# Performance work log

Hardware: AMD Instinct MI355X
Metric: run time of the kernel (lower is better)

Reference implementation:

```python
import jax, jax.numpy as jnp
import numpy as np

B, C, H, W = 16, 256, 32, 32
LN_EPS = 1e-5


def setup_inputs() -> dict:
    key = jax.random.key(0)
    ks = jax.random.split(key, 12)
    s = 1.0 / np.sqrt(C)
    x = jax.random.normal(ks[0], (B, C, H, W), dtype=jnp.float32)
    # Linear weights stored as [in, out] (torch stores [out, in]; math is x @ W_in_out + b)
    wq = jax.random.uniform(ks[1], (C, C), jnp.float32, -s, s)
    bq = jax.random.uniform(ks[2], (C,), jnp.float32, -s, s)
    wk = jax.random.uniform(ks[3], (C, C), jnp.float32, -s, s)
    bk = jax.random.uniform(ks[4], (C,), jnp.float32, -s, s)
    wv = jax.random.uniform(ks[5], (C, C), jnp.float32, -s, s)
    bv = jax.random.uniform(ks[6], (C,), jnp.float32, -s, s)
    w1 = jax.random.uniform(ks[7], (C, C), jnp.float32, -s, s)
    b1 = jax.random.uniform(ks[8], (C,), jnp.float32, -s, s)
    w2 = jax.random.uniform(ks[9], (C, C), jnp.float32, -s, s)
    b2 = jax.random.uniform(ks[10], (C,), jnp.float32, -s, s)
    gamma = jnp.ones((C,), jnp.float32)
    beta = jnp.zeros((C,), jnp.float32)
    return {"x": x, "wq": wq, "bq": bq, "wk": wk, "bk": bk, "wv": wv, "bv": bv,
            "w1": w1, "b1": b1, "w2": w2, "b2": b2, "gamma": gamma, "beta": beta}


def reference(x, wq, bq, wk, bk, wv, bv, w1, b1, w2, b2, gamma, beta):
    Bd, Cd, Hd, Wd = x.shape
    t = x.reshape(Bd, Cd, Hd * Wd).transpose(0, 2, 1)  # [B, N, C]
    q = t @ wq + bq
    k = t @ wk + bk
    v = t @ wv + bv
    # matrix[b,i,j] = q[b,i,:] . k[b,j,:]  (no 1/sqrt(d) scaling, as in source)
    m = jnp.einsum('bic,bjc->bij', q, k)
    # softmax over dim=-2 (the query axis i)
    m = jax.nn.softmax(m, axis=-2)
    # att[b,j,c] = sum_i v[b,i,c] * m[b,i,j]  (v^T @ m, then permute)
    att = jnp.einsum('bic,bij->bjc', v, m)  # [B, N, C]
    # MLP (SiLU, hidden = C), dropout p=0 -> identity; DropPath eval -> identity
    att = jax.nn.silu(att @ w1 + b1) @ w2 + b2
    # LayerNorm over channel dim
    mu = jnp.mean(att, axis=-1, keepdims=True)
    var = jnp.var(att, axis=-1, keepdims=True)
    att = (att - mu) * jax.lax.rsqrt(var + LN_EPS) * gamma + beta
    return att.transpose(0, 2, 1).reshape(Bd, Cd, Hd, Wd)
```

## Files before the change

### kernel.cpp

```cpp
#include <hip/hip_runtime.h>

#define BB 16
#define CC 256
#define NN 1024

typedef _Float16 f16;
typedef __attribute__((ext_vector_type(8))) _Float16 half8;
typedef __attribute__((ext_vector_type(4))) float f32x4;

__device__ __forceinline__ half8 ldg8(const f16* p) {
  return *reinterpret_cast<const half8*>(p);
}

__device__ __forceinline__ void gll16(const f16* g, f16* l) {
  __builtin_amdgcn_global_load_lds((const __attribute__((address_space(1))) void*)g,
                                   (__attribute__((address_space(3))) void*)l, 16, 0, 0);
}

#define VMCNT(n) asm volatile("s_waitcnt vmcnt(" #n ")" ::: "memory")
#define BAR() __builtin_amdgcn_s_barrier()

__device__ __forceinline__ void stage64k(const f16* __restrict__ g, f16* l, int wave, int lane) {
#pragma unroll
  for (int k = 0; k < 16; ++k) {
    int ob = k * 2048 + wave * 512;
    gll16(g + ob + lane * 8, l + ob);
  }
}

__device__ __forceinline__ void stage64k8(const f16* __restrict__ g, f16* l, int wave, int lane) {
#pragma unroll
  for (int k = 0; k < 8; ++k) {
    int ob = k * 4096 + wave * 512;
    gll16(g + ob + lane * 8, l + ob);
  }
}

struct WP5 {
  const float* s[5];
  f16* d[5];
};

__global__ void __launch_bounds__(256) k_packW(WP5 p) {
  __shared__ float ws[256][17];
  int m = blockIdx.y, ct = blockIdx.x;
  const float* W = p.s[m];
  f16* wp = p.d[m];
  int tid = threadIdx.x;
  int col = tid & 15, cig = tid >> 4;
#pragma unroll
  for (int pg = 0; pg < 16; ++pg) {
    int ci = pg * 16 + cig;
    ws[ci][col] = W[(size_t)ci * 256 + ct * 16 + col];
  }
  __syncthreads();
  int lane = tid & 63, wave = tid >> 6;
  int row16 = lane & 15, quad = lane >> 4;
#pragma unroll
  for (int kk = 0; kk < 2; ++kk) {
    int kc = wave * 2 + kk;
    half8 o;
#pragma unroll
    for (int j = 0; j < 8; ++j) o[j] = (f16)ws[kc * 32 + quad * 8 + j][row16];
    *reinterpret_cast<half8*>(wp + ((size_t)ct * 8 + kc) * 512 + lane * 8) = o;
  }
}

struct QkvSmem {
  union {
    struct { f16 hi[32][264]; f16 lo[32][264]; } ts;
    f16 ex[2][16][264];
    f16 exv[256][40];
  };
};

__global__ void __launch_bounds__(256) k_qkv(const float* __restrict__ x,
    const f16* __restrict__ wqp, const f16* __restrict__ wkp, const f16* __restrict__ wvp,
    const float* __restrict__ bq, const float* __restrict__ bk, const float* __restrict__ bv,
    f16* __restrict__ qp, f16* __restrict__ kp, f16* __restrict__ vp, int b_base) {
  __shared__ QkvSmem sm;
  int bl = blockIdx.x, bg = b_base + bl, n0 = blockIdx.y * 32;
  int tid = threadIdx.x, wave = tid >> 6, lane = tid & 63;
  int row16 = lane & 15, quad = lane >> 4;
  int g = wave >> 1, h = wave & 1;

#pragma unroll
  for (int e = tid; e < 2048; e += 256) {
    int c = e >> 3, n4 = (e & 7) << 2;
    float4 u = *reinterpret_cast<const float4*>(x + (size_t)(bg * CC + c) * NN + n0 + n4);
    float uv[4] = {u.x, u.y, u.z, u.w};
#pragma unroll
    for (int i = 0; i < 4; ++i) {
      f16 hh = (f16)uv[i];
      sm.ts.hi[n4 + i][c] = hh;
      sm.ts.lo[n4 + i][c] = (f16)(uv[i] - (float)hh);
    }
  }
  __syncthreads();

  half8 ah[8], al[8];
#pragma unroll
  for (int kc = 0; kc < 8; ++kc) {
    ah[kc] = *reinterpret_cast<const half8*>(&sm.ts.hi[g * 16 + row16][kc * 32 + quad * 8]);
    al[kc] = *reinterpret_cast<const half8*>(&sm.ts.lo[g * 16 + row16][kc * 32 + quad * 8]);
  }
  __syncthreads();

  const f16* WTs[2]    = {wqp, wkp};
  const float* biases[2] = {bq, bk};
  f16* outs[2]         = {qp, kp};
#pragma unroll
  for (int z = 0; z < 2; ++z) {
    const f16* WT = WTs[z];
    const float* bias = biases[z];
    f16* outp = outs[z];
#pragma unroll
    for (int cp = 0; cp < 2; ++cp) {
      f32x4 acch[4], accl[4];
#pragma unroll
      for (int u = 0; u < 4; ++u) { acch[u] = {0.f,0.f,0.f,0.f}; accl[u] = {0.f,0.f,0.f,0.f}; }
#pragma unroll
      for (int kc = 0; kc < 8; ++kc) {
#pragma unroll
        for (int u = 0; u < 4; ++u) {
          int ct = h * 8 + cp * 4 + u;
          half8 b = ldg8(WT + ((size_t)ct * 8 + kc) * 512 + lane * 8);
          acch[u] = __builtin_amdgcn_mfma_f32_16x16x32_f16(ah[kc], b, acch[u], 0, 0, 0);
          accl[u] = __builtin_amdgcn_mfma_f32_16x16x32_f16(al[kc], b, accl[u], 0, 0, 0);
        }
      }
#pragma unroll
      for (int u = 0; u < 4; ++u) {
        int ct = h * 8 + cp * 4 + u;
        int co = ct * 16 + row16;
        float bb = bias[co];
#pragma unroll
        for (int r = 0; r < 4; ++r)
          sm.ex[g][quad * 4 + r][co] = (f16)(acch[u][r] + accl[u][r] + bb);
      }
    }
    const f16* exr = &sm.ex[g][row16][0];
    size_t fb = ((size_t)bl * 64 + (n0 >> 4) + g) * 8;
#pragma unroll
    for (int k = 0; k < 4; ++k) {
      int kc = h * 4 + k;
      half8 hv = *reinterpret_cast<const half8*>(exr + kc * 32 + quad * 8);
      *reinterpret_cast<half8*>(outp + (fb + kc) * 512 + lane * 8) = hv;
    }
  }
  __syncthreads();

#pragma unroll
  for (int cp = 0; cp < 2; ++cp) {
    f32x4 acch[4], accl[4];
#pragma unroll
    for (int u = 0; u < 4; ++u) { acch[u] = {0.f,0.f,0.f,0.f}; accl[u] = {0.f,0.f,0.f,0.f}; }
#pragma unroll
    for (int kc = 0; kc < 8; ++kc) {
#pragma unroll
      for (int u = 0; u < 4; ++u) {
        int ct = h * 8 + cp * 4 + u;
        half8 b = ldg8(wvp + ((size_t)ct * 8 + kc) * 512 + lane * 8);
        acch[u] = __builtin_amdgcn_mfma_f32_16x16x32_f16(ah[kc], b, acch[u], 0, 0, 0);
        accl[u] = __builtin_amdgcn_mfma_f32_16x16x32_f16(al[kc], b, accl[u], 0, 0, 0);
      }
    }
#pragma unroll
    for (int u = 0; u < 4; ++u) {
      int ct = h * 8 + cp * 4 + u;
      int co = ct * 16 + row16;
      float bb = bv[co];
#pragma unroll
      for (int r = 0; r < 4; ++r)
        sm.exv[co][g * 16 + quad * 4 + r] = (f16)(acch[u][r] + accl[u][r] + bb);
    }
  }
  __syncthreads();
  size_t vb = ((size_t)bl * 32 + blockIdx.y) * 16;
#pragma unroll
  for (int f = 0; f < 4; ++f) {
    int ct = wave * 4 + f;
    half8 o = *reinterpret_cast<const half8*>(&sm.exv[ct * 16 + row16][quad * 8]);
    *reinterpret_cast<half8*>(vp + (vb + ct) * 512 + lane * 8) = o;
  }
}

struct AttnSmem {
  union {
    struct {
      f16 QB[2][64 * 256];
      f16 VB[2][64 * 256];
    } s;
    struct {
      union {
        float Ocmb[4][16][260];
        f16 ex2[4][16][264];
      } a;
      f16 ex[4][16][264];
    } e;
  } u;
  f16 P[8][2][16][40];
  float ml[8][2][16];
  float lnbuf[8][2][16];
};

__global__ void __launch_bounds__(512, 2) k_attn_mlp(
    const f16* __restrict__ qp, const f16* __restrict__ kp, const f16* __restrict__ vp,
    const f16* __restrict__ w1p, const float* __restrict__ b1,
    const f16* __restrict__ w2p, const float* __restrict__ b2,
    const float* __restrict__ gamma, const float* __restrict__ beta,
    float* __restrict__ out, int b_base) {
  __shared__ AttnSmem sm;
  int bl = blockIdx.x, bg = b_base + bl;
  int j0 = blockIdx.y * 64;
  int tid = threadIdx.x, wave = tid >> 6, lane = tid & 63;
  int row16 = lane & 15, quad = lane >> 4;
  int jt_l = wave & 3, p = wave >> 2;
  int jw = j0 + jt_l * 16;

  const f16* kbase = kp + (size_t)bl * NN * CC;
  int jt = (j0 >> 4) + jt_l;
  half8 kf[8];
#pragma unroll
  for (int kc = 0; kc < 8; ++kc)
    kf[kc] = ldg8(kbase + ((size_t)jt * 8 + kc) * 512 + lane * 8);

  const f16* qbase = qp + (size_t)bl * NN * CC;
  const f16* vbase = vp + (size_t)bl * CC * NN;

  stage64k8(qbase, &sm.u.s.QB[0][0], wave, lane);
  stage64k8(vbase, &sm.u.s.VB[0][0], wave, lane);
  VMCNT(8);
  BAR();

  f32x4 O[16];
#pragma unroll
  for (int ct = 0; ct < 16; ++ct) O[ct] = {0.f, 0.f, 0.f, 0.f};
  float m_run[4], l_lane[4];
#pragma unroll
  for (int r = 0; r < 4; ++r) { m_run[r] = -1e30f; l_lane[r] = 0.f; }

  const f16* QBp = &sm.u.s.QB[p][0];
  const f16* VBp = &sm.u.s.VB[p][0];

  for (int it = 0; it < 8; ++it) {
    f32x4 s[4];
#pragma unroll
    for (int f = 0; f < 4; ++f) s[f] = {0.f, 0.f, 0.f, 0.f};
#pragma unroll
    for (int kc = 0; kc < 8; ++kc) {
#pragma unroll
      for (int f = 0; f < 4; ++f) {
        half8 b = *reinterpret_cast<const half8*>(&QBp[(f * 8 + kc) * 512 + lane * 8]);
        s[f] = __builtin_amdgcn_mfma_f32_16x16x32_f16(kf[kc], b, s[f], 0, 0, 0);
      }
    }
    BAR();
    stage64k8(qbase + (size_t)((it + 1) & 7) * 32768, &sm.u.s.QB[0][0], wave, lane);

    float alpha[4];
#pragma unroll
    for (int r = 0; r < 4; ++r) {
      float mx = s[0][r];
#pragma unroll
      for (int f = 1; f < 4; ++f) mx = fmaxf(mx, s[f][r]);
#pragma unroll
      for (int off = 1; off < 16; off <<= 1) mx = fmaxf(mx, __shfl_xor(mx, off, 64));
      float mnew = fmaxf(m_run[r], mx);
      alpha[r] = __expf(m_run[r] - mnew);
      m_run[r] = mnew;
      float ps = 0.f;
#pragma unroll
      for (int f = 0; f < 4; ++f) {
        float pv = __expf(s[f][r] - mnew);
        ps += pv;
        sm.P[wave][f >> 1][quad * 4 + r][(f & 1) * 16 + row16] = (f16)pv;
      }
      l_lane[r] = l_lane[r] * alpha[r] + ps;
    }
#pragma unroll
    for (int ct = 0; ct < 16; ++ct)
#pragma unroll
      for (int r = 0; r < 4; ++r) O[ct][r] *= alpha[r];

    VMCNT(8);
    BAR();

#pragma unroll
    for (int c4 = 0; c4 < 2; ++c4) {
      half8 pf = *reinterpret_cast<const half8*>(&sm.P[wave][c4][row16][quad * 8]);
#pragma unroll
      for (int ct = 0; ct < 16; ++ct) {
        half8 vf = *reinterpret_cast<const half8*>(&VBp[(c4 * 16 + ct) * 512 + lane * 8]);
        O[ct] = __builtin_amdgcn_mfma_f32_16x16x32_f16(pf, vf, O[ct], 0, 0, 0);
      }
    }
    BAR();
    stage64k8(vbase + (size_t)((it + 1) & 7) * 32768, &sm.u.s.VB[0][0], wave, lane);
    VMCNT(8);
    BAR();
  }
  VMCNT(0);
  BAR();

#pragma unroll
  for (int r = 0; r < 4; ++r) {
#pragma unroll
    for (int off = 1; off < 16; off <<= 1) l_lane[r] += __shfl_xor(l_lane[r], off, 64);
  }
  if (row16 == 0) {
#pragma unroll
    for (int r = 0; r < 4; ++r) {
      sm.ml[wave][0][quad * 4 + r] = m_run[r];
      sm.ml[wave][1][quad * 4 + r] = l_lane[r];
    }
  }
  BAR();

  int partner = wave ^ 4;
  float alphaS[4], invL[4];
#pragma unroll
  for (int r = 0; r < 4; ++r) {
    int j = quad * 4 + r;
    float ma = m_run[r], mb = sm.ml[partner][0][j];
    float M = fmaxf(ma, mb);
    float la = l_lane[r], lb = sm.ml[partner][1][j];
    float L = la * __expf(ma - M) + lb * __expf(mb - M);
    alphaS[r] = __expf(ma - M);
    invL[r] = 1.f / L;
  }
#pragma unroll
  for (int ct = 0; ct < 16; ++ct)
#pragma unroll
    for (int r = 0; r < 4; ++r) O[ct][r] *= alphaS[r];

  if (p == 1) {
#pragma unroll
    for (int ct = 0; ct < 16; ++ct)
#pragma unroll
      for (int r = 0; r < 4; ++r)
        sm.u.e.a.Ocmb[jt_l][quad * 4 + r][ct * 16 + row16] = O[ct][r];
  }
  BAR();
  if (p == 0) {
#pragma unroll
    for (int ct = 0; ct < 16; ++ct)
#pragma unroll
      for (int r = 0; r < 4; ++r) {
        float v = O[ct][r] + sm.u.e.a.Ocmb[jt_l][quad * 4 + r][ct * 16 + row16];
        sm.u.e.ex[jt_l][quad * 4 + r][ct * 16 + row16] = (f16)(v * invL[r]);
      }
  }
  BAR();

  half8 af[8];
#pragma unroll
  for (int kc = 0; kc < 8; ++kc)
    af[kc] = *reinterpret_cast<const half8*>(&sm.u.e.ex[jt_l][row16][kc * 32 + quad * 8]);

#pragma unroll
  for (int q8 = 0; q8 < 8; ++q8) {
    int ct = p * 8 + q8;
    f32x4 acc = {0.f, 0.f, 0.f, 0.f};
    const f16* brow = w1p + ((size_t)ct * 8) * 512 + lane * 8;
#pragma unroll
    for (int kc = 0; kc < 8; ++kc)
      acc = __builtin_amdgcn_mfma_f32_16x16x32_f16(af[kc], ldg8(brow + kc * 512), acc, 0, 0, 0);
    int co = ct * 16 + row16;
    float bb = b1[co];
#pragma unroll
    for (int r = 0; r < 4; ++r) {
      float xg = acc[r] + bb;
      float hh = xg / (1.f + __expf(-xg));
      sm.u.e.a.ex2[jt_l][quad * 4 + r][co] = (f16)hh;
    }
  }
  BAR();

  half8 hf[8];
#pragma unroll
  for (int kc = 0; kc < 8; ++kc)
    hf[kc] = *reinterpret_cast<const half8*>(&sm.u.e.a.ex2[jt_l][row16][kc * 32 + quad * 8]);

  f32x4 acc2[8];
#pragma unroll
  for (int q8 = 0; q8 < 8; ++q8) {
    int ct = p * 8 + q8;
    f32x4 acc = {0.f, 0.f, 0.f, 0.f};
    const f16* brow = w2p + ((size_t)ct * 8) * 512 + lane * 8;
#pragma unroll
    for (int kc = 0; kc < 8; ++kc)
      acc = __builtin_amdgcn_mfma_f32_16x16x32_f16(hf[kc], ldg8(brow + kc * 512), acc, 0, 0, 0);
    float bb = b2[ct * 16 + row16];
#pragma unroll
    for (int r = 0; r < 4; ++r) acc[r] += bb;
    acc2[q8] = acc;
  }

  float sum[4] = {0.f, 0.f, 0.f, 0.f}, ssq[4] = {0.f, 0.f, 0.f, 0.f};
#pragma unroll
  for (int q8 = 0; q8 < 8; ++q8)
#pragma unroll
    for (int r = 0; r < 4; ++r) { float xv = acc2[q8][r]; sum[r] += xv; ssq[r] += xv * xv; }
#pragma unroll
  for (int r = 0; r < 4; ++r) {
#pragma unroll
    for (int off = 1; off < 16; off <<= 1) {
      sum[r] += __shfl_xor(sum[r], off, 64);
      ssq[r] += __shfl_xor(ssq[r], off, 64);
    }
  }
  if (row16 == 0) {
#pragma unroll
    for (int r = 0; r < 4; ++r) {
      sm.lnbuf[wave][0][quad * 4 + r] = sum[r];
      sm.lnbuf[wave][1][quad * 4 + r] = ssq[r];
    }
  }
  BAR();

  float mean[4], rstd[4];
#pragma unroll
  for (int r = 0; r < 4; ++r) {
    int j = quad * 4 + r;
    float s = sm.lnbuf[wave][0][j] + sm.lnbuf[partner][0][j];
    float sq = sm.lnbuf[wave][1][j] + sm.lnbuf[partner][1][j];
    mean[r] = s * (1.f / 256.f);
    float var = sq * (1.f / 256.f) - mean[r] * mean[r];
    rstd[r] = rsqrtf(var + 1e-5f);
  }

#pragma unroll
  for (int q8 = 0; q8 < 8; ++q8) {
    int col = (p * 8 + q8) * 16 + row16;
    float g = gamma[col], be = beta[col];
    f32x4 v;
#pragma unroll
    for (int r = 0; r < 4; ++r) v[r] = (acc2[q8][r] - mean[r]) * rstd[r] * g + be;
    __builtin_nontemporal_store(v,
        reinterpret_cast<f32x4*>(out + (size_t)(bg * CC + col) * NN + jw + quad * 4));
  }
}

extern "C" void kernel_launch(void* const* d_in, const int* in_sizes, int n_in,
                              void* d_out, int out_size, void* d_ws, size_t ws_size,
                              hipStream_t stream) {
  (void)in_sizes; (void)n_in; (void)out_size;
  const float* x     = (const float*)d_in[0];
  const float* wq    = (const float*)d_in[1];
  const float* bq    = (const float*)d_in[2];
  const float* wk    = (const float*)d_in[3];
  const float* bk    = (const float*)d_in[4];
  const float* wv    = (const float*)d_in[5];
  const float* bv    = (const float*)d_in[6];
  const float* w1    = (const float*)d_in[7];
  const float* b1    = (const float*)d_in[8];
  const float* w2    = (const float*)d_in[9];
  const float* b2    = (const float*)d_in[10];
  const float* gamma = (const float*)d_in[11];
  const float* beta  = (const float*)d_in[12];
  float* out = (float*)d_out;

  const size_t WE = 65536;
  const size_t SB = (size_t)NN * CC;
  f16* base = (f16*)d_ws;
  f16* wqp = base + 0 * WE;
  f16* wkp = base + 1 * WE;
  f16* wvp = base + 2 * WE;
  f16* w1p = base + 3 * WE;
  f16* w2p = base + 4 * WE;

  size_t wbytes = 5 * WE * sizeof(f16);
  size_t perb   = 3 * SB * sizeof(f16);
  int nb = (ws_size > wbytes) ? (int)((ws_size - wbytes) / perb) : 1;
  if (nb < 1) nb = 1;
  if (nb > BB) nb = BB;

  f16* qb  = base + 5 * WE;
  f16* kb  = qb + (size_t)nb * SB;
  f16* vTb = kb + (size_t)nb * SB;

  WP5 p;
  p.s[0] = wq; p.s[1] = wk; p.s[2] = wv; p.s[3] = w1; p.s[4] = w2;
  p.d[0] = wqp; p.d[1] = wkp; p.d[2] = wvp; p.d[3] = w1p; p.d[4] = w2p;
  k_packW<<<dim3(16, 5), 256, 0, stream>>>(p);

  for (int b0 = 0; b0 < BB; b0 += nb) {
    int cb = (b0 + nb <= BB) ? nb : (BB - b0);
    k_qkv<<<dim3(cb, 32), 256, 0, stream>>>(x, wqp, wkp, wvp, bq, bk, bv, qb, kb, vTb, b0);
    k_attn_mlp<<<dim3(cb, 16), 512, 0, stream>>>(qb, kb, vTb, w1p, b1, w2p, b2,
                                                 gamma, beta, out, b0);
  }
}
```

Measured before the change: 176.6 us.

## Split attention key loop across four wave groups in 1024-thread blocks

The attention/MLP kernel now runs 16 waves per block instead of 8. Each group of four waves handles a quarter of each 128-query chunk instead of half. The partial softmax states are merged across four groups through sequential shared-memory accumulation, and the MLP output columns are split four ways. This aims to raise per-CU wave parallelism and cut per-wave MFMA work, at the cost of more barriers, serialized reduction phases, and losing the two-blocks-per-CU launch bound.

```diff
diff --git a/kernel.cpp b/kernel.cpp
--- a/kernel.cpp
+++ b/kernel.cpp
@@ -20,18 +20,10 @@
 #define VMCNT(n) asm volatile("s_waitcnt vmcnt(" #n ")" ::: "memory")
 #define BAR() __builtin_amdgcn_s_barrier()
 
-__device__ __forceinline__ void stage64k(const f16* __restrict__ g, f16* l, int wave, int lane) {
-#pragma unroll
-  for (int k = 0; k < 16; ++k) {
-    int ob = k * 2048 + wave * 512;
-    gll16(g + ob + lane * 8, l + ob);
-  }
-}
-
-__device__ __forceinline__ void stage64k8(const f16* __restrict__ g, f16* l, int wave, int lane) {
-#pragma unroll
-  for (int k = 0; k < 8; ++k) {
-    int ob = k * 4096 + wave * 512;
+__device__ __forceinline__ void stage64k16(const f16* __restrict__ g, f16* l, int wave, int lane) {
+#pragma unroll
+  for (int k = 0; k < 4; ++k) {
+    int ob = k * 8192 + wave * 512;
     gll16(g + ob + lane * 8, l + ob);
   }
 }
@@ -188,23 +180,20 @@
 struct AttnSmem {
   union {
     struct {
-      f16 QB[2][64 * 256];
-      f16 VB[2][64 * 256];
+      f16 QB[128 * 256];
+      f16 VB[128 * 256];
     } s;
     struct {
-      union {
-        float Ocmb[4][16][260];
-        f16 ex2[4][16][264];
-      } a;
+      float Ocmb[4][16][260];
       f16 ex[4][16][264];
     } e;
   } u;
-  f16 P[8][2][16][40];
-  float ml[8][2][16];
-  float lnbuf[8][2][16];
+  f16 P[16][16][40];
+  float ml[16][2][16];
+  float lnbuf[16][2][16];
 };
 
-__global__ void __launch_bounds__(512, 2) k_attn_mlp(
+__global__ void __launch_bounds__(1024) k_attn_mlp(
     const f16* __restrict__ qp, const f16* __restrict__ kp, const f16* __restrict__ vp,
     const f16* __restrict__ w1p, const float* __restrict__ b1,
     const f16* __restrict__ w2p, const float* __restrict__ b2,
@@ -228,9 +217,9 @@
   const f16* qbase = qp + (size_t)bl * NN * CC;
   const f16* vbase = vp + (size_t)bl * CC * NN;
 
-  stage64k8(qbase, &sm.u.s.QB[0][0], wave, lane);
-  stage64k8(vbase, &sm.u.s.VB[0][0], wave, lane);
-  VMCNT(8);
+  stage64k16(qbase, sm.u.s.QB, wave, lane);
+  stage64k16(vbase, sm.u.s.VB, wave, lane);
+  VMCNT(4);
   BAR();
 
   f32x4 O[16];
@@ -240,30 +229,28 @@
 #pragma unroll
   for (int r = 0; r < 4; ++r) { m_run[r] = -1e30f; l_lane[r] = 0.f; }
 
-  const f16* QBp = &sm.u.s.QB[p][0];
-  const f16* VBp = &sm.u.s.VB[p][0];
+  const f16* QBp = &sm.u.s.QB[p * 8192];
+  const f16* VBp = &sm.u.s.VB[p * 8192];
 
   for (int it = 0; it < 8; ++it) {
-    f32x4 s[4];
-#pragma unroll
-    for (int f = 0; f < 4; ++f) s[f] = {0.f, 0.f, 0.f, 0.f};
+    f32x4 s[2];
+#pragma unroll
+    for (int f = 0; f < 2; ++f) s[f] = {0.f, 0.f, 0.f, 0.f};
 #pragma unroll
     for (int kc = 0; kc < 8; ++kc) {
 #pragma unroll
-      for (int f = 0; f < 4; ++f) {
+      for (int f = 0; f < 2; ++f) {
         half8 b = *reinterpret_cast<const half8*>(&QBp[(f * 8 + kc) * 512 + lane * 8]);
         s[f] = __builtin_amdgcn_mfma_f32_16x16x32_f16(kf[kc], b, s[f], 0, 0, 0);
       }
     }
     BAR();
-    stage64k8(qbase + (size_t)((it + 1) & 7) * 32768, &sm.u.s.QB[0][0], wave, lane);
+    stage64k16(qbase + (size_t)((it + 1) & 7) * 32768, sm.u.s.QB, wave, lane);
 
     float alpha[4];
 #pragma unroll
     for (int r = 0; r < 4; ++r) {
-      float mx = s[0][r];
-#pragma unroll
-      for (int f = 1; f < 4; ++f) mx = fmaxf(mx, s[f][r]);
+      float mx = fmaxf(s[0][r], s[1][r]);
 #pragma unroll
       for (int off = 1; off < 16; off <<= 1) mx = fmaxf(mx, __shfl_xor(mx, off, 64));
       float mnew = fmaxf(m_run[r], mx);
@@ -271,10 +258,10 @@
       m_run[r] = mnew;
       float ps = 0.f;
 #pragma unroll
-      for (int f = 0; f < 4; ++f) {
+      for (int f = 0; f < 2; ++f) {
         float pv = __expf(s[f][r] - mnew);
         ps += pv;
-        sm.P[wave][f >> 1][quad * 4 + r][(f & 1) * 16 + row16] = (f16)pv;
+        sm.P[wave][quad * 4 + r][f * 16 + row16] = (f16)pv;
       }
       l_lane[r] = l_lane[r] * alpha[r] + ps;
     }
@@ -283,21 +270,20 @@
 #pragma unroll
       for (int r = 0; r < 4; ++r) O[ct][r] *= alpha[r];
 
-    VMCNT(8);
+    VMCNT(4);
     BAR();
 
-#pragma unroll
-    for (int c4 = 0; c4 < 2; ++c4) {
-      half8 pf = *reinterpret_cast<const half8*>(&sm.P[wave][c4][row16][quad * 8]);
+    {
+      half8 pf = *reinterpret_cast<const half8*>(&sm.P[wave][row16][quad * 8]);
 #pragma unroll
       for (int ct = 0; ct < 16; ++ct) {
-        half8 vf = *reinterpret_cast<const half8*>(&VBp[(c4 * 16 + ct) * 512 + lane * 8]);
+        half8 vf = *reinterpret_cast<const half8*>(&VBp[ct * 512 + lane * 8]);
         O[ct] = __builtin_amdgcn_mfma_f32_16x16x32_f16(pf, vf, O[ct], 0, 0, 0);
       }
     }
     BAR();
-    stage64k8(vbase + (size_t)((it + 1) & 7) * 32768, &sm.u.s.VB[0][0], wave, lane);
-    VMCNT(8);
+    stage64k16(vbase + (size_t)((it + 1) & 7) * 32768, sm.u.s.VB, wave, lane);
+    VMCNT(4);
     BAR();
   }
   VMCNT(0);
@@ -317,37 +303,51 @@
   }
   BAR();
 
-  int partner = wave ^ 4;
-  float alphaS[4], invL[4];
+  float aS[4], invL[4];
 #pragma unroll
   for (int r = 0; r < 4; ++r) {
     int j = quad * 4 + r;
-    float ma = m_run[r], mb = sm.ml[partner][0][j];
-    float M = fmaxf(ma, mb);
-    float la = l_lane[r], lb = sm.ml[partner][1][j];
-    float L = la * __expf(ma - M) + lb * __expf(mb - M);
-    alphaS[r] = __expf(ma - M);
+    float M = sm.ml[jt_l][0][j];
+#pragma unroll
+    for (int w4 = 1; w4 < 4; ++w4) M = fmaxf(M, sm.ml[jt_l + w4 * 4][0][j]);
+    float L = 0.f;
+#pragma unroll
+    for (int w4 = 0; w4 < 4; ++w4)
+      L += sm.ml[jt_l + w4 * 4][1][j] * __expf(sm.ml[jt_l + w4 * 4][0][j] - M);
+    aS[r] = __expf(m_run[r] - M);
     invL[r] = 1.f / L;
   }
-#pragma unroll
-  for (int ct = 0; ct < 16; ++ct)
-#pragma unroll
-    for (int r = 0; r < 4; ++r) O[ct][r] *= alphaS[r];
-
+
+  if (p == 0) {
+#pragma unroll
+    for (int ct = 0; ct < 16; ++ct)
+#pragma unroll
+      for (int r = 0; r < 4; ++r)
+        sm.u.e.Ocmb[jt_l][quad * 4 + r][ct * 16 + row16] = O[ct][r] * aS[r];
+  }
+  BAR();
   if (p == 1) {
 #pragma unroll
     for (int ct = 0; ct < 16; ++ct)
 #pragma unroll
       for (int r = 0; r < 4; ++r)
-        sm.u.e.a.Ocmb[jt_l][quad * 4 + r][ct * 16 + row16] = O[ct][r];
-  }
-  BAR();
-  if (p == 0) {
+        sm.u.e.Ocmb[jt_l][quad * 4 + r][ct * 16 + row16] += O[ct][r] * aS[r];
+  }
+  BAR();
+  if (p == 2) {
 #pragma unroll
     for (int ct = 0; ct < 16; ++ct)
 #pragma unroll
+      for (int r = 0; r < 4; ++r)
+        sm.u.e.Ocmb[jt_l][quad * 4 + r][ct * 16 + row16] += O[ct][r] * aS[r];
+  }
+  BAR();
+  if (p == 3) {
+#pragma unroll
+    for (int ct = 0; ct < 16; ++ct)
+#pragma unroll
       for (int r = 0; r < 4; ++r) {
-        float v = O[ct][r] + sm.u.e.a.Ocmb[jt_l][quad * 4 + r][ct * 16 + row16];
+        float v = sm.u.e.Ocmb[jt_l][quad * 4 + r][ct * 16 + row16] + O[ct][r] * aS[r];
         sm.u.e.ex[jt_l][quad * 4 + r][ct * 16 + row16] = (f16)(v * invL[r]);
       }
   }
@@ -357,10 +357,11 @@
 #pragma unroll
   for (int kc = 0; kc < 8; ++kc)
     af[kc] = *reinterpret_cast<const half8*>(&sm.u.e.ex[jt_l][row16][kc * 32 + quad * 8]);
-
-#pragma unroll
-  for (int q8 = 0; q8 < 8; ++q8) {
-    int ct = p * 8 + q8;
+  BAR();
+
+#pragma unroll
+  for (int q = 0; q < 4; ++q) {
+    int ct = p * 4 + q;
     f32x4 acc = {0.f, 0.f, 0.f, 0.f};
     const f16* brow = w1p + ((size_t)ct * 8) * 512 + lane * 8;
 #pragma unroll
@@ -372,7 +373,7 @@
     for (int r = 0; r < 4; ++r) {
       float xg = acc[r] + bb;
       float hh = xg / (1.f + __expf(-xg));
-      sm.u.e.a.ex2[jt_l][quad * 4 + r][co] = (f16)hh;
+      sm.u.e.ex[jt_l][quad * 4 + r][co] = (f16)hh;
     }
   }
   BAR();
@@ -380,12 +381,12 @@
   half8 hf[8];
 #pragma unroll
   for (int kc = 0; kc < 8; ++kc)
-    hf[kc] = *reinterpret_cast<const half8*>(&sm.u.e.a.ex2[jt_l][row16][kc * 32 + quad * 8]);
-
-  f32x4 acc2[8];
-#pragma unroll
-  for (int q8 = 0; q8 < 8; ++q8) {
-    int ct = p * 8 + q8;
+    hf[kc] = *reinterpret_cast<const half8*>(&sm.u.e.ex[jt_l][row16][kc * 32 + quad * 8]);
+
+  f32x4 acc2[4];
+#pragma unroll
+  for (int q = 0; q < 4; ++q) {
+    int ct = p * 4 + q;
     f32x4 acc = {0.f, 0.f, 0.f, 0.f};
     const f16* brow = w2p + ((size_t)ct * 8) * 512 + lane * 8;
 #pragma unroll
@@ -394,14 +395,14 @@
     float bb = b2[ct * 16 + row16];
 #pragma unroll
     for (int r = 0; r < 4; ++r) acc[r] += bb;
-    acc2[q8] = acc;
+    acc2[q] = acc;
   }
 
   float sum[4] = {0.f, 0.f, 0.f, 0.f}, ssq[4] = {0.f, 0.f, 0.f, 0.f};
 #pragma unroll
-  for (int q8 = 0; q8 < 8; ++q8)
-#pragma unroll
-    for (int r = 0; r < 4; ++r) { float xv = acc2[q8][r]; sum[r] += xv; ssq[r] += xv * xv; }
+  for (int q = 0; q < 4; ++q)
+#pragma unroll
+    for (int r = 0; r < 4; ++r) { float xv = acc2[q][r]; sum[r] += xv; ssq[r] += xv * xv; }
 #pragma unroll
   for (int r = 0; r < 4; ++r) {
 #pragma unroll
@@ -423,22 +424,25 @@
 #pragma unroll
   for (int r = 0; r < 4; ++r) {
     int j = quad * 4 + r;
-    float s = sm.lnbuf[wave][0][j] + sm.lnbuf[partner][0][j];
-    float sq = sm.lnbuf[wave][1][j] + sm.lnbuf[partner][1][j];
+    float s = 0.f, sq = 0.f;
+#pragma unroll
+    for (int w4 = 0; w4 < 4; ++w4) {
+      s  += sm.lnbuf[jt_l + w4 * 4][0][j];
+      sq += sm.lnbuf[jt_l + w4 * 4][1][j];
+    }
     mean[r] = s * (1.f / 256.f);
     float var = sq * (1.f / 256.f) - mean[r] * mean[r];
     rstd[r] = rsqrtf(var + 1e-5f);
   }
 
 #pragma unroll
-  for (int q8 = 0; q8 < 8; ++q8) {
-    int col = (p * 8 + q8) * 16 + row16;
+  for (int q = 0; q < 4; ++q) {
+    int col = (p * 4 + q) * 16 + row16;
     float g = gamma[col], be = beta[col];
     f32x4 v;
 #pragma unroll
-    for (int r = 0; r < 4; ++r) v[r] = (acc2[q8][r] - mean[r]) * rstd[r] * g + be;
-    __builtin_nontemporal_store(v,
-        reinterpret_cast<f32x4*>(out + (size_t)(bg * CC + col) * NN + jw + quad * 4));
+    for (int r = 0; r < 4; ++r) v[r] = (acc2[q][r] - mean[r]) * rstd[r] * g + be;
+    *reinterpret_cast<f32x4*>(out + (size_t)(bg * CC + col) * NN + jw + quad * 4) = v;
   }
 }
 
@@ -488,7 +492,7 @@
   for (int b0 = 0; b0 < BB; b0 += nb) {
     int cb = (b0 + nb <= BB) ? nb : (BB - b0);
     k_qkv<<<dim3(cb, 32), 256, 0, stream>>>(x, wqp, wkp, wvp, bq, bk, bv, qb, kb, vTb, b0);
-    k_attn_mlp<<<dim3(cb, 16), 512, 0, stream>>>(qb, kb, vTb, w1p, b1, w2p, b2,
-                                                 gamma, beta, out, b0);
-  }
-}
+    k_attn_mlp<<<dim3(cb, 16), 1024, 0, stream>>>(qb, kb, vTb, w1p, b1, w2p, b2,
+                                                  gamma, beta, out, b0);
+  }
+}
```

Measured after the change: 209.8 us. +18.8%, slower.

## Halve attention KV staging tile to shrink shared memory and split the O-combine

Applied to the files above, without the earlier changes.

Each iteration of the attention loop now stages 32 query/value rows instead of 64, doubling the trip count to 16 and halving the QB/VB buffers and the P scratch. The cross-half O reduction is done in two passes of 8 column tiles through a smaller Ocmb buffer, which is reused for the MLP hidden buffer. The aim is to cut LDS use so that more blocks fit per CU. The cost is more barriers and more staging rounds per block. The final output store also changes from a nontemporal store to a plain store.

```diff
diff --git a/kernel.cpp b/kernel.cpp
--- a/kernel.cpp
+++ b/kernel.cpp
@@ -20,17 +20,9 @@
 #define VMCNT(n) asm volatile("s_waitcnt vmcnt(" #n ")" ::: "memory")
 #define BAR() __builtin_amdgcn_s_barrier()
 
-__device__ __forceinline__ void stage64k(const f16* __restrict__ g, f16* l, int wave, int lane) {
-#pragma unroll
-  for (int k = 0; k < 16; ++k) {
-    int ob = k * 2048 + wave * 512;
-    gll16(g + ob + lane * 8, l + ob);
-  }
-}
-
-__device__ __forceinline__ void stage64k8(const f16* __restrict__ g, f16* l, int wave, int lane) {
-#pragma unroll
-  for (int k = 0; k < 8; ++k) {
+__device__ __forceinline__ void stage32k8(const f16* __restrict__ g, f16* l, int wave, int lane) {
+#pragma unroll
+  for (int k = 0; k < 4; ++k) {
     int ob = k * 4096 + wave * 512;
     gll16(g + ob + lane * 8, l + ob);
   }
@@ -188,18 +180,15 @@
 struct AttnSmem {
   union {
     struct {
-      f16 QB[2][64 * 256];
-      f16 VB[2][64 * 256];
+      f16 QB[64 * 256];
+      f16 VB[64 * 256];
     } s;
     struct {
-      union {
-        float Ocmb[4][16][260];
-        f16 ex2[4][16][264];
-      } a;
+      float Ocmb[4][16][132];
       f16 ex[4][16][264];
     } e;
   } u;
-  f16 P[8][2][16][40];
+  f16 P[8][16][40];
   float ml[8][2][16];
   float lnbuf[8][2][16];
 };
@@ -228,9 +217,9 @@
   const f16* qbase = qp + (size_t)bl * NN * CC;
   const f16* vbase = vp + (size_t)bl * CC * NN;
 
-  stage64k8(qbase, &sm.u.s.QB[0][0], wave, lane);
-  stage64k8(vbase, &sm.u.s.VB[0][0], wave, lane);
-  VMCNT(8);
+  stage32k8(qbase, sm.u.s.QB, wave, lane);
+  stage32k8(vbase, sm.u.s.VB, wave, lane);
+  VMCNT(4);
   BAR();
 
   f32x4 O[16];
@@ -240,30 +229,28 @@
 #pragma unroll
   for (int r = 0; r < 4; ++r) { m_run[r] = -1e30f; l_lane[r] = 0.f; }
 
-  const f16* QBp = &sm.u.s.QB[p][0];
-  const f16* VBp = &sm.u.s.VB[p][0];
-
-  for (int it = 0; it < 8; ++it) {
-    f32x4 s[4];
-#pragma unroll
-    for (int f = 0; f < 4; ++f) s[f] = {0.f, 0.f, 0.f, 0.f};
+  const f16* QBp = &sm.u.s.QB[p * 8192];
+  const f16* VBp = &sm.u.s.VB[p * 8192];
+
+  for (int it = 0; it < 16; ++it) {
+    f32x4 s[2];
+#pragma unroll
+    for (int f = 0; f < 2; ++f) s[f] = {0.f, 0.f, 0.f, 0.f};
 #pragma unroll
     for (int kc = 0; kc < 8; ++kc) {
 #pragma unroll
-      for (int f = 0; f < 4; ++f) {
+      for (int f = 0; f < 2; ++f) {
         half8 b = *reinterpret_cast<const half8*>(&QBp[(f * 8 + kc) * 512 + lane * 8]);
         s[f] = __builtin_amdgcn_mfma_f32_16x16x32_f16(kf[kc], b, s[f], 0, 0, 0);
       }
     }
     BAR();
-    stage64k8(qbase + (size_t)((it + 1) & 7) * 32768, &sm.u.s.QB[0][0], wave, lane);
+    stage32k8(qbase + (size_t)((it + 1) & 15) * 16384, sm.u.s.QB, wave, lane);
 
     float alpha[4];
 #pragma unroll
     for (int r = 0; r < 4; ++r) {
-      float mx = s[0][r];
-#pragma unroll
-      for (int f = 1; f < 4; ++f) mx = fmaxf(mx, s[f][r]);
+      float mx = fmaxf(s[0][r], s[1][r]);
 #pragma unroll
       for (int off = 1; off < 16; off <<= 1) mx = fmaxf(mx, __shfl_xor(mx, off, 64));
       float mnew = fmaxf(m_run[r], mx);
@@ -271,10 +258,10 @@
       m_run[r] = mnew;
       float ps = 0.f;
 #pragma unroll
-      for (int f = 0; f < 4; ++f) {
+      for (int f = 0; f < 2; ++f) {
         float pv = __expf(s[f][r] - mnew);
         ps += pv;
-        sm.P[wave][f >> 1][quad * 4 + r][(f & 1) * 16 + row16] = (f16)pv;
+        sm.P[wave][quad * 4 + r][f * 16 + row16] = (f16)pv;
       }
       l_lane[r] = l_lane[r] * alpha[r] + ps;
     }
@@ -283,21 +270,20 @@
 #pragma unroll
       for (int r = 0; r < 4; ++r) O[ct][r] *= alpha[r];
 
-    VMCNT(8);
+    VMCNT(4);
     BAR();
 
-#pragma unroll
-    for (int c4 = 0; c4 < 2; ++c4) {
-      half8 pf = *reinterpret_cast<const half8*>(&sm.P[wave][c4][row16][quad * 8]);
+    {
+      half8 pf = *reinterpret_cast<const half8*>(&sm.P[wave][row16][quad * 8]);
 #pragma unroll
       for (int ct = 0; ct < 16; ++ct) {
-        half8 vf = *reinterpret_cast<const half8*>(&VBp[(c4 * 16 + ct) * 512 + lane * 8]);
+        half8 vf = *reinterpret_cast<const half8*>(&VBp[ct * 512 + lane * 8]);
         O[ct] = __builtin_amdgcn_mfma_f32_16x16x32_f16(pf, vf, O[ct], 0, 0, 0);
       }
     }
     BAR();
-    stage64k8(vbase + (size_t)((it + 1) & 7) * 32768, &sm.u.s.VB[0][0], wave, lane);
-    VMCNT(8);
+    stage32k8(vbase + (size_t)((it + 1) & 15) * 16384, sm.u.s.VB, wave, lane);
+    VMCNT(4);
     BAR();
   }
   VMCNT(0);
@@ -318,36 +304,53 @@
   BAR();
 
   int partner = wave ^ 4;
-  float alphaS[4], invL[4];
+  float aS[4], invL[4];
 #pragma unroll
   for (int r = 0; r < 4; ++r) {
     int j = quad * 4 + r;
     float ma = m_run[r], mb = sm.ml[partner][0][j];
     float M = fmaxf(ma, mb);
-    float la = l_lane[r], lb = sm.ml[partner][1][j];
-    float L = la * __expf(ma - M) + lb * __expf(mb - M);
-    alphaS[r] = __expf(ma - M);
+    float L = l_lane[r] * __expf(ma - M) + sm.ml[partner][1][j] * __expf(mb - M);
+    aS[r] = __expf(ma - M);
     invL[r] = 1.f / L;
   }
 #pragma unroll
   for (int ct = 0; ct < 16; ++ct)
 #pragma unroll
-    for (int r = 0; r < 4; ++r) O[ct][r] *= alphaS[r];
-
+    for (int r = 0; r < 4; ++r) O[ct][r] *= aS[r];
+
+  if (p == 0) {
+#pragma unroll
+    for (int ct = 0; ct < 8; ++ct)
+#pragma unroll
+      for (int r = 0; r < 4; ++r)
+        sm.u.e.Ocmb[jt_l][quad * 4 + r][ct * 16 + row16] = O[ct][r];
+  }
+  BAR();
   if (p == 1) {
 #pragma unroll
-    for (int ct = 0; ct < 16; ++ct)
+    for (int ct = 0; ct < 8; ++ct)
+#pragma unroll
+      for (int r = 0; r < 4; ++r) {
+        float v = sm.u.e.Ocmb[jt_l][quad * 4 + r][ct * 16 + row16] + O[ct][r];
+        sm.u.e.ex[jt_l][quad * 4 + r][ct * 16 + row16] = (f16)(v * invL[r]);
+      }
+  }
+  BAR();
+  if (p == 0) {
+#pragma unroll
+    for (int ct = 8; ct < 16; ++ct)
 #pragma unroll
       for (int r = 0; r < 4; ++r)
-        sm.u.e.a.Ocmb[jt_l][quad * 4 + r][ct * 16 + row16] = O[ct][r];
-  }
-  BAR();
-  if (p == 0) {
-#pragma unroll
-    for (int ct = 0; ct < 16; ++ct)
+        sm.u.e.Ocmb[jt_l][quad * 4 + r][(ct - 8) * 16 + row16] = O[ct][r];
+  }
+  BAR();
+  if (p == 1) {
+#pragma unroll
+    for (int ct = 8; ct < 16; ++ct)
 #pragma unroll
       for (int r = 0; r < 4; ++r) {
-        float v = O[ct][r] + sm.u.e.a.Ocmb[jt_l][quad * 4 + r][ct * 16 + row16];
+        float v = sm.u.e.Ocmb[jt_l][quad * 4 + r][(ct - 8) * 16 + row16] + O[ct][r];
         sm.u.e.ex[jt_l][quad * 4 + r][ct * 16 + row16] = (f16)(v * invL[r]);
       }
   }
@@ -357,6 +360,8 @@
 #pragma unroll
   for (int kc = 0; kc < 8; ++kc)
     af[kc] = *reinterpret_cast<const half8*>(&sm.u.e.ex[jt_l][row16][kc * 32 + quad * 8]);
+
+  f16* ex2 = reinterpret_cast<f16*>(&sm.u.e.Ocmb[0][0][0]);
 
 #pragma unroll
   for (int q8 = 0; q8 < 8; ++q8) {
@@ -372,7 +377,7 @@
     for (int r = 0; r < 4; ++r) {
       float xg = acc[r] + bb;
       float hh = xg / (1.f + __expf(-xg));
-      sm.u.e.a.ex2[jt_l][quad * 4 + r][co] = (f16)hh;
+      ex2[((size_t)jt_l * 16 + quad * 4 + r) * 264 + co] = (f16)hh;
     }
   }
   BAR();
@@ -380,7 +385,7 @@
   half8 hf[8];
 #pragma unroll
   for (int kc = 0; kc < 8; ++kc)
-    hf[kc] = *reinterpret_cast<const half8*>(&sm.u.e.a.ex2[jt_l][row16][kc * 32 + quad * 8]);
+    hf[kc] = *reinterpret_cast<const half8*>(&ex2[((size_t)jt_l * 16 + row16) * 264 + kc * 32 + quad * 8]);
 
   f32x4 acc2[8];
 #pragma unroll
@@ -423,7 +428,7 @@
 #pragma unroll
   for (int r = 0; r < 4; ++r) {
     int j = quad * 4 + r;
-    float s = sm.lnbuf[wave][0][j] + sm.lnbuf[partner][0][j];
+    float s  = sm.lnbuf[wave][0][j] + sm.lnbuf[partner][0][j];
     float sq = sm.lnbuf[wave][1][j] + sm.lnbuf[partner][1][j];
     mean[r] = s * (1.f / 256.f);
     float var = sq * (1.f / 256.f) - mean[r] * mean[r];
@@ -437,8 +442,7 @@
     f32x4 v;
 #pragma unroll
     for (int r = 0; r < 4; ++r) v[r] = (acc2[q8][r] - mean[r]) * rstd[r] * g + be;
-    __builtin_nontemporal_store(v,
-        reinterpret_cast<f32x4*>(out + (size_t)(bg * CC + col) * NN + jw + quad * 4));
+    *reinterpret_cast<f32x4*>(out + (size_t)(bg * CC + col) * NN + jw + quad * 4) = v;
   }
 }
 
```

New measurement: 187.5 us. 1.06x slower.

## Split QKV projection across grid z into Q/K and V blocks

Applied to the files above, without the earlier changes.

The QKV kernel grid gains a z dimension of 2: z=0 blocks compute Q and K, z=1 blocks compute V. This doubles the block count so more CUs have work. The accumulator working set is halved and launch bounds ask for 4 blocks per CU to raise occupancy. The cost is that each block converts and loads its x tile into LDS, so x is read and split twice. Separately, the final output store switches from a nontemporal store to a normal store, and an unused staging helper is removed.

```diff
diff --git a/kernel.cpp b/kernel.cpp
--- a/kernel.cpp
+++ b/kernel.cpp
@@ -19,14 +19,6 @@
 
 #define VMCNT(n) asm volatile("s_waitcnt vmcnt(" #n ")" ::: "memory")
 #define BAR() __builtin_amdgcn_s_barrier()
-
-__device__ __forceinline__ void stage64k(const f16* __restrict__ g, f16* l, int wave, int lane) {
-#pragma unroll
-  for (int k = 0; k < 16; ++k) {
-    int ob = k * 2048 + wave * 512;
-    gll16(g + ob + lane * 8, l + ob);
-  }
-}
 
 __device__ __forceinline__ void stage64k8(const f16* __restrict__ g, f16* l, int wave, int lane) {
 #pragma unroll
@@ -74,11 +66,12 @@
   };
 };
 
-__global__ void __launch_bounds__(256) k_qkv(const float* __restrict__ x,
+__global__ void __launch_bounds__(256, 4) k_qkv(const float* __restrict__ x,
     const f16* __restrict__ wqp, const f16* __restrict__ wkp, const f16* __restrict__ wvp,
     const float* __restrict__ bq, const float* __restrict__ bk, const float* __restrict__ bv,
     f16* __restrict__ qp, f16* __restrict__ kp, f16* __restrict__ vp, int b_base) {
   __shared__ QkvSmem sm;
+  int z = blockIdx.z;
   int bl = blockIdx.x, bg = b_base + bl, n0 = blockIdx.y * 32;
   int tid = threadIdx.x, wave = tid >> 6, lane = tid & 63;
   int row16 = lane & 15, quad = lane >> 4;
@@ -106,82 +99,89 @@
   }
   __syncthreads();
 
-  const f16* WTs[2]    = {wqp, wkp};
-  const float* biases[2] = {bq, bk};
-  f16* outs[2]         = {qp, kp};
-#pragma unroll
-  for (int z = 0; z < 2; ++z) {
-    const f16* WT = WTs[z];
-    const float* bias = biases[z];
-    f16* outp = outs[z];
+  if (z == 0) {
+    const f16* WTs[2]      = {wqp, wkp};
+    const float* biases[2] = {bq, bk};
+    f16* outs[2]           = {qp, kp};
+#pragma unroll
+    for (int zz = 0; zz < 2; ++zz) {
+      const f16* WT = WTs[zz];
+      const float* bias = biases[zz];
+      f16* outp = outs[zz];
+#pragma unroll
+      for (int cp = 0; cp < 2; ++cp) {
+#pragma unroll
+        for (int uu = 0; uu < 2; ++uu) {
+          f32x4 acch[2], accl[2];
+#pragma unroll
+          for (int u = 0; u < 2; ++u) { acch[u] = {0.f,0.f,0.f,0.f}; accl[u] = {0.f,0.f,0.f,0.f}; }
+#pragma unroll
+          for (int kc = 0; kc < 8; ++kc) {
+#pragma unroll
+            for (int u = 0; u < 2; ++u) {
+              int ct = h * 8 + cp * 4 + uu * 2 + u;
+              half8 b = ldg8(WT + ((size_t)ct * 8 + kc) * 512 + lane * 8);
+              acch[u] = __builtin_amdgcn_mfma_f32_16x16x32_f16(ah[kc], b, acch[u], 0, 0, 0);
+              accl[u] = __builtin_amdgcn_mfma_f32_16x16x32_f16(al[kc], b, accl[u], 0, 0, 0);
+            }
+          }
+#pragma unroll
+          for (int u = 0; u < 2; ++u) {
+            int ct = h * 8 + cp * 4 + uu * 2 + u;
+            int co = ct * 16 + row16;
+            float bb = bias[co];
+#pragma unroll
+            for (int r = 0; r < 4; ++r)
+              sm.ex[g][quad * 4 + r][co] = (f16)(acch[u][r] + accl[u][r] + bb);
+          }
+        }
+      }
+      const f16* exr = &sm.ex[g][row16][0];
+      size_t fb = ((size_t)bl * 64 + (n0 >> 4) + g) * 8;
+#pragma unroll
+      for (int k = 0; k < 4; ++k) {
+        int kc = h * 4 + k;
+        half8 hv = *reinterpret_cast<const half8*>(exr + kc * 32 + quad * 8);
+        *reinterpret_cast<half8*>(outp + (fb + kc) * 512 + lane * 8) = hv;
+      }
+    }
+  } else {
 #pragma unroll
     for (int cp = 0; cp < 2; ++cp) {
-      f32x4 acch[4], accl[4];
-#pragma unroll
-      for (int u = 0; u < 4; ++u) { acch[u] = {0.f,0.f,0.f,0.f}; accl[u] = {0.f,0.f,0.f,0.f}; }
-#pragma unroll
-      for (int kc = 0; kc < 8; ++kc) {
-#pragma unroll
-        for (int u = 0; u < 4; ++u) {
-          int ct = h * 8 + cp * 4 + u;
-          half8 b = ldg8(WT + ((size_t)ct * 8 + kc) * 512 + lane * 8);
-          acch[u] = __builtin_amdgcn_mfma_f32_16x16x32_f16(ah[kc], b, acch[u], 0, 0, 0);
-          accl[u] = __builtin_amdgcn_mfma_f32_16x16x32_f16(al[kc], b, accl[u], 0, 0, 0);
+#pragma unroll
+      for (int uu = 0; uu < 2; ++uu) {
+        f32x4 acch[2], accl[2];
+#pragma unroll
+        for (int u = 0; u < 2; ++u) { acch[u] = {0.f,0.f,0.f,0.f}; accl[u] = {0.f,0.f,0.f,0.f}; }
+#pragma unroll
+        for (int kc = 0; kc < 8; ++kc) {
+#pragma unroll
+          for (int u = 0; u < 2; ++u) {
+            int ct = h * 8 + cp * 4 + uu * 2 + u;
+            half8 b = ldg8(wvp + ((size_t)ct * 8 + kc) * 512 + lane * 8);
+            acch[u] = __builtin_amdgcn_mfma_f32_16x16x32_f16(ah[kc], b, acch[u], 0, 0, 0);
+            accl[u] = __builtin_amdgcn_mfma_f32_16x16x32_f16(al[kc], b, accl[u], 0, 0, 0);
+          }
         }
-      }
-#pragma unroll
-      for (int u = 0; u < 4; ++u) {
-        int ct = h * 8 + cp * 4 + u;
-        int co = ct * 16 + row16;
-        float bb = bias[co];
-#pragma unroll
-        for (int r = 0; r < 4; ++r)
-          sm.ex[g][quad * 4 + r][co] = (f16)(acch[u][r] + accl[u][r] + bb);
-      }
-    }
-    const f16* exr = &sm.ex[g][row16][0];
-    size_t fb = ((size_t)bl * 64 + (n0 >> 4) + g) * 8;
-#pragma unroll
-    for (int k = 0; k < 4; ++k) {
-      int kc = h * 4 + k;
-      half8 hv = *reinterpret_cast<const half8*>(exr + kc * 32 + quad * 8);
-      *reinterpret_cast<half8*>(outp + (fb + kc) * 512 + lane * 8) = hv;
-    }
-  }
-  __syncthreads();
-
-#pragma unroll
-  for (int cp = 0; cp < 2; ++cp) {
-    f32x4 acch[4], accl[4];
-#pragma unroll
-    for (int u = 0; u < 4; ++u) { acch[u] = {0.f,0.f,0.f,0.f}; accl[u] = {0.f,0.f,0.f,0.f}; }
-#pragma unroll
-    for (int kc = 0; kc < 8; ++kc) {
-#pragma unroll
-      for (int u = 0; u < 4; ++u) {
-        int ct = h * 8 + cp * 4 + u;
-        half8 b = ldg8(wvp + ((size_t)ct * 8 + kc) * 512 + lane * 8);
-        acch[u] = __builtin_amdgcn_mfma_f32_16x16x32_f16(ah[kc], b, acch[u], 0, 0, 0);
-        accl[u] = __builtin_amdgcn_mfma_f32_16x16x32_f16(al[kc], b, accl[u], 0, 0, 0);
-      }
-    }
-#pragma unroll
-    for (int u = 0; u < 4; ++u) {
-      int ct = h * 8 + cp * 4 + u;
-      int co = ct * 16 + row16;
-      float bb = bv[co];
-#pragma unroll
-      for (int r = 0; r < 4; ++r)
-        sm.exv[co][g * 16 + quad * 4 + r] = (f16)(acch[u][r] + accl[u][r] + bb);
-    }
-  }
-  __syncthreads();
-  size_t vb = ((size_t)bl * 32 + blockIdx.y) * 16;
-#pragma unroll
-  for (int f = 0; f < 4; ++f) {
-    int ct = wave * 4 + f;
-    half8 o = *reinterpret_cast<const half8*>(&sm.exv[ct * 16 + row16][quad * 8]);
-    *reinterpret_cast<half8*>(vp + (vb + ct) * 512 + lane * 8) = o;
+#pragma unroll
+        for (int u = 0; u < 2; ++u) {
+          int ct = h * 8 + cp * 4 + uu * 2 + u;
+          int co = ct * 16 + row16;
+          float bb = bv[co];
+#pragma unroll
+          for (int r = 0; r < 4; ++r)
+            sm.exv[co][g * 16 + quad * 4 + r] = (f16)(acch[u][r] + accl[u][r] + bb);
+        }
+      }
+    }
+    __syncthreads();
+    size_t vb = ((size_t)bl * 32 + blockIdx.y) * 16;
+#pragma unroll
+    for (int f = 0; f < 4; ++f) {
+      int ct = wave * 4 + f;
+      half8 o = *reinterpret_cast<const half8*>(&sm.exv[ct * 16 + row16][quad * 8]);
+      *reinterpret_cast<half8*>(vp + (vb + ct) * 512 + lane * 8) = o;
+    }
   }
 }
 
@@ -437,8 +437,7 @@
     f32x4 v;
 #pragma unroll
     for (int r = 0; r < 4; ++r) v[r] = (acc2[q8][r] - mean[r]) * rstd[r] * g + be;
-    __builtin_nontemporal_store(v,
-        reinterpret_cast<f32x4*>(out + (size_t)(bg * CC + col) * NN + jw + quad * 4));
+    *reinterpret_cast<f32x4*>(out + (size_t)(bg * CC + col) * NN + jw + quad * 4) = v;
   }
 }
 
@@ -487,7 +486,7 @@
 
   for (int b0 = 0; b0 < BB; b0 += nb) {
     int cb = (b0 + nb <= BB) ? nb : (BB - b0);
-    k_qkv<<<dim3(cb, 32), 256, 0, stream>>>(x, wqp, wkp, wvp, bq, bk, bv, qb, kb, vTb, b0);
+    k_qkv<<<dim3(cb, 32, 2), 256, 0, stream>>>(x, wqp, wkp, wvp, bq, bk, bv, qb, kb, vTb, b0);
     k_attn_mlp<<<dim3(cb, 16), 512, 0, stream>>>(qb, kb, vTb, w1p, b1, w2p, b2,
                                                  gamma, beta, out, b0);
   }
```

After: 183.3 us. +3.8%, slower.
